# Kernel optimization log

Measured on AMD Instinct MI355X. Metric: run time of the kernel, lower is better.

Reference implementation:

```python
import jax, jax.numpy as jnp
import numpy as np

B = 4096
D_INPUT = 20
CTX = 10
IN_DIM = CTX * (D_INPUT + 1) + D_INPUT  # 230
D_MODEL = 256
N_LAYERS = 12
D_STATE = 16
D_CONV = 4
EXPAND = 2
D_INNER = EXPAND * D_MODEL  # 512
DT_RANK = (D_MODEL + 15) // 16  # ceil(256/16) = 16


def setup_inputs() -> dict:
    key = jax.random.key(0)
    ks = jax.random.split(key, 12)
    s = lambda k, shape, scale=0.02: jax.random.normal(k, shape, jnp.float32) * scale
    A = jnp.broadcast_to(jnp.arange(1, D_STATE + 1, dtype=jnp.float32), (N_LAYERS, D_INNER, D_STATE))
    return {
        "x": jax.random.normal(ks[0], (B, IN_DIM), jnp.float32),
        "Wi": s(ks[1], (IN_DIM, D_MODEL)),
        "bi": jnp.zeros((D_MODEL,), jnp.float32),
        "in_proj_w": s(ks[2], (N_LAYERS, D_MODEL, 2 * D_INNER)),
        "conv_w": s(ks[3], (N_LAYERS, D_INNER, D_CONV), 0.3),
        "conv_b": jnp.zeros((N_LAYERS, D_INNER), jnp.float32),
        "x_proj_w": s(ks[4], (N_LAYERS, D_INNER, DT_RANK + 2 * D_STATE)),
        "dt_proj_w": s(ks[5], (N_LAYERS, DT_RANK, D_INNER), 0.1),
        "dt_proj_b": jnp.full((N_LAYERS, D_INNER), -4.6, jnp.float32),  # softplus -> small dt
        "A_log": jnp.log(A),  # S4D-real init as in mamba_ssm
        "D": jnp.ones((N_LAYERS, D_INNER), jnp.float32),
        "out_proj_w": s(ks[6], (N_LAYERS, D_INNER, D_MODEL)),
        "Wo": s(ks[7], (D_MODEL, 1)),
        "bo": jnp.zeros((1,), jnp.float32),
    }


def _mamba_block(h, in_proj, conv_w, conv_b, x_proj, dt_w, dt_b, A_log, Dp, out_proj):
    # h: (B, L, D_MODEL)
    Bn, L, _ = h.shape
    xz = h @ in_proj                       # (B, L, 2*D_INNER)
    xr, z = jnp.split(xz, 2, axis=-1)
    # causal depthwise conv1d, kernel D_CONV, left-pad D_CONV-1
    xp = jnp.pad(xr, ((0, 0), (D_CONV - 1, 0), (0, 0)))
    win = jnp.stack([xp[:, k:k + L, :] for k in range(D_CONV)], axis=-1)  # (B,L,C,K)
    xc = jnp.einsum('blck,ck->blc', win, conv_w) + conv_b
    xc = jax.nn.silu(xc)
    dbl = xc @ x_proj                      # (B, L, DT_RANK + 2*D_STATE)
    dt, Bm, Cm = jnp.split(dbl, [DT_RANK, DT_RANK + D_STATE], axis=-1)
    dt = jax.nn.softplus(dt @ dt_w + dt_b)  # (B, L, D_INNER)
    A = -jnp.exp(A_log)                     # (D_INNER, D_STATE)
    dA = jnp.exp(dt[..., None] * A)                              # (B,L,di,ds)
    dBu = dt[..., None] * Bm[:, :, None, :] * xc[..., None]      # (B,L,di,ds)

    def step(hs, inp):
        dA_t, dBu_t, C_t = inp
        hs = dA_t * hs + dBu_t             # (B, di, ds)
        y_t = jnp.einsum('bds,bs->bd', hs, C_t)
        return hs, y_t

    h0 = jnp.zeros((Bn, D_INNER, D_STATE), h.dtype)
    _, ys = jax.lax.scan(step, h0, (dA.swapaxes(0, 1), dBu.swapaxes(0, 1), Cm.swapaxes(0, 1)))
    y = ys.swapaxes(0, 1)                  # (B, L, D_INNER)
    y = y + xc * Dp
    y = y * jax.nn.silu(z)
    return y @ out_proj                    # (B, L, D_MODEL)


def reference(x, Wi, bi, in_proj_w, conv_w, conv_b, x_proj_w, dt_proj_w, dt_proj_b, A_log, D, out_proj_w, Wo, bo):
    h = (x @ Wi + bi)[:, None, :]          # (B, 1, D_MODEL) -- unsqueeze(1)
    for i in range(N_LAYERS):
        h = _mamba_block(h, in_proj_w[i], conv_w[i], conv_b[i], x_proj_w[i],
                         dt_proj_w[i], dt_proj_b[i], A_log[i], D[i], out_proj_w[i])
    h = h[:, 0, :]                         # squeeze(1)
    return h @ Wo + bo                     # (B, 1)
```

## Files before the change

kernel.cpp:

```cpp
#include <hip/hip_runtime.h>
#include <hip/hip_fp8.h>
#include <math.h>

#define NB 4096
#define IN_D 230
#define DM 256
#define NL 12
#define DST 16
#define DI 512
#define DTR 16
#define XPN 48
#define XB 528
#define HB 272

typedef __attribute__((ext_vector_type(4))) float floatx4;
typedef __attribute__((ext_vector_type(2))) float floatx2;
typedef __attribute__((ext_vector_type(2))) long long2v;
typedef __attribute__((ext_vector_type(4))) int intx4;
typedef __attribute__((ext_vector_type(8))) int intx8;

__device__ __forceinline__ float silu_f(float x) {
    return x * __builtin_amdgcn_rcpf(1.0f + __expf(-x));
}
__device__ __forceinline__ float softplus_f(float x) {
    return (x > 20.0f) ? x : __logf(1.0f + __expf(x));
}

__device__ __forceinline__ unsigned char f2fp8(float x) {
#if __has_builtin(__builtin_amdgcn_cvt_pk_fp8_f32)
    return (unsigned char)(__builtin_amdgcn_cvt_pk_fp8_f32(x, x, 0, false) & 0xff);
#else
    __hip_fp8_e4m3 t(x); return (unsigned char)t.__x;
#endif
}
__device__ __forceinline__ unsigned pk4fp8(float a, float b, float c, float d) {
    unsigned w = __builtin_amdgcn_cvt_pk_fp8_f32(a, b, 0, false);
    return __builtin_amdgcn_cvt_pk_fp8_f32(c, d, w, true);
}
template<int S>
__device__ __forceinline__ float fp8sel(unsigned w) {
    return __builtin_amdgcn_cvt_f32_fp8((int)w, S);
}

__device__ __forceinline__ unsigned f2fp4(float x) {
    float ax = fabsf(x);
    unsigned s = (x < 0.0f) ? 8u : 0u;
    unsigned m;
    if      (ax < 0.25f) m = 0;
    else if (ax < 0.75f) m = 1;
    else if (ax < 1.25f) m = 2;
    else if (ax < 1.75f) m = 3;
    else if (ax < 2.50f) m = 4;
    else if (ax < 3.50f) m = 5;
    else if (ax < 5.00f) m = 6;
    else                 m = 7;
    return s | m;
}

__global__ __launch_bounds__(256) void pack_all(
    const float* __restrict__ x,
    const float* __restrict__ Wi, const float* __restrict__ ip,
    const float* __restrict__ op, const float* __restrict__ xp,
    const float* __restrict__ dtw,
    const float* __restrict__ cw, const float* __restrict__ cb,
    const float* __restrict__ db, const float* __restrict__ Dv,
    unsigned char* __restrict__ xpad,
    unsigned char* __restrict__ WiT, unsigned char* __restrict__ dtwP,
    unsigned char* __restrict__ ip4, unsigned char* __restrict__ op4,
    unsigned char* __restrict__ xp4,
    floatx2* __restrict__ cwcb, floatx2* __restrict__ dbdv)
{
    __shared__ float tbuf[64][65];
    const int fid = blockIdx.x;

    if (fid < 1264) {
        const float* src; unsigned char* dst;
        int K, N, ngK, t;
        bool isfp4;
        if (fid < 16) {
            src = Wi; dst = WiT; K = IN_D; N = DM; ngK = 4; t = fid; isfp4 = false;
        } else if (fid < 784) {
            int local = fid - 16; int l = local >> 6; t = local & 63;
            K = DM; N = 2 * DI; ngK = 4; isfp4 = true;
            src = ip + (size_t)l * K * N; dst = ip4 + (size_t)l * 131072;
        } else if (fid < 1168) {
            int local = fid - 784; int l = local >> 5; t = local & 31;
            K = DI; N = DM; ngK = 8; isfp4 = true;
            src = op + (size_t)l * K * N; dst = op4 + (size_t)l * 65536;
        } else {
            int local = fid - 1168; int l = local >> 3; t = local & 7;
            K = DI; N = XPN; ngK = 8; isfp4 = true;
            src = xp + (size_t)l * K * N; dst = xp4 + (size_t)l * 16384;
        }
        const int g = t % ngK, nb = t / ngK;
        const int k0 = g * 64, n0 = nb * 64;
        {
            const int r = threadIdx.x >> 6, c = threadIdx.x & 63;
#pragma unroll
            for (int i = 0; i < 16; i++) {
                int kk = k0 + i * 4 + r;
                int nn = n0 + c;
                tbuf[i * 4 + r][c] = (kk < K && nn < N) ? src[(size_t)kk * N + nn] : 0.0f;
            }
        }
        __syncthreads();
        if (!isfp4) {
            const int cbi = threadIdx.x >> 6;
            const int lane = threadIdx.x & 63;
            const int q = lane >> 4, m16 = lane & 15;
            const int chunk = (nb * 4 + cbi) * ngK + g;
            union { unsigned char b[16]; intx4 v; } buf;
#pragma unroll
            for (int sub = 0; sub < 2; sub++)
#pragma unroll
                for (int byt = 0; byt < 8; byt++) {
                    int k = sub * 32 + q * 8 + byt;
                    int n = cbi * 16 + m16;
                    buf.b[sub * 8 + byt] = f2fp8(tbuf[k][n]);
                }
            *(intx4*)(dst + (size_t)chunk * 1024 + lane * 16) = buf.v;
        } else {
            const int kg = g >> 1, half = g & 1;
            const int nkg128 = ngK >> 1;
            const int cbi = threadIdx.x >> 6;
            const int rem = threadIdx.x & 63;
            const int q4loc = rem >> 5;
            const int hb = (rem >> 4) & 1;
            const int m16 = rem & 15;
            const int q4 = half * 2 + q4loc;
            const int chunk = (nb * 4 + cbi) * nkg128 + kg;
            const int kb = q4loc * 32 + hb * 16;
            const int nn = cbi * 16 + m16;
            union { unsigned u[2]; long v; } buf;
#if __has_builtin(__builtin_amdgcn_cvt_scalef32_pk_fp4_f32)
            unsigned d0 = 0, d1 = 0;
            d0 = __builtin_amdgcn_cvt_scalef32_pk_fp4_f32(d0, tbuf[kb + 0][nn] * 128.0f, tbuf[kb + 1][nn] * 128.0f, 1.0f, 0);
            d0 = __builtin_amdgcn_cvt_scalef32_pk_fp4_f32(d0, tbuf[kb + 2][nn] * 128.0f, tbuf[kb + 3][nn] * 128.0f, 1.0f, 1);
            d0 = __builtin_amdgcn_cvt_scalef32_pk_fp4_f32(d0, tbuf[kb + 4][nn] * 128.0f, tbuf[kb + 5][nn] * 128.0f, 1.0f, 2);
            d0 = __builtin_amdgcn_cvt_scalef32_pk_fp4_f32(d0, tbuf[kb + 6][nn] * 128.0f, tbuf[kb + 7][nn] * 128.0f, 1.0f, 3);
            d1 = __builtin_amdgcn_cvt_scalef32_pk_fp4_f32(d1, tbuf[kb + 8][nn] * 128.0f, tbuf[kb + 9][nn] * 128.0f, 1.0f, 0);
            d1 = __builtin_amdgcn_cvt_scalef32_pk_fp4_f32(d1, tbuf[kb + 10][nn] * 128.0f, tbuf[kb + 11][nn] * 128.0f, 1.0f, 1);
            d1 = __builtin_amdgcn_cvt_scalef32_pk_fp4_f32(d1, tbuf[kb + 12][nn] * 128.0f, tbuf[kb + 13][nn] * 128.0f, 1.0f, 2);
            d1 = __builtin_amdgcn_cvt_scalef32_pk_fp4_f32(d1, tbuf[kb + 14][nn] * 128.0f, tbuf[kb + 15][nn] * 128.0f, 1.0f, 3);
            buf.u[0] = d0; buf.u[1] = d1;
#else
            union { unsigned char b[8]; long v; } bb;
#pragma unroll
            for (int bl = 0; bl < 8; bl++) {
                unsigned ob = 0;
#pragma unroll
                for (int i = 0; i < 2; i++) {
                    float v = tbuf[kb + bl * 2 + i][nn] * 128.0f;
                    ob |= f2fp4(v) << (i * 4);
                }
                bb.b[bl] = (unsigned char)ob;
            }
            buf.v = bb.v;
#endif
            *(long*)(dst + (size_t)chunk * 1024 + (q4 * 16 + m16) * 16 + hb * 8) = buf.v;
        }
    } else if (fid < 1456) {
        int gid = (fid - 1264) * 256 + threadIdx.x;
        int idx = gid * 4;
        int l = idx >> 14;
        int r14 = idx & 16383;
        int chunk = r14 >> 9;
        int rr = r14 & 511;
        int lane = rr >> 3, byt0 = rr & 7;
        int q = lane >> 4, m16 = lane & 15;
        int col = chunk * 16 + m16;
        float v[4];
#pragma unroll
        for (int j = 0; j < 4; j++) {
            int k = q * 8 + byt0 + j;
            v[j] = (k < DTR) ? dtw[(size_t)l * DTR * DI + (size_t)k * DI + col] : 0.0f;
        }
        *(unsigned*)(dtwP + idx) = pk4fp8(v[0], v[1], v[2], v[3]);
    } else if (fid < 1480) {
        int idx = (fid - 1456) * 256 + threadIdx.x;
        floatx2 v; v.x = cw[(size_t)idx * 4 + 3]; v.y = cb[idx];
        cwcb[idx] = v;
    } else if (fid < 1504) {
        int idx = (fid - 1480) * 256 + threadIdx.x;
        floatx2 v; v.x = db[idx]; v.y = Dv[idx];
        dbdv[idx] = v;
    } else {
        int gid = (fid - 1504) * 256 + threadIdx.x;
        int r = gid >> 6, c4 = (gid & 63) * 4;
        float v[4];
#pragma unroll
        for (int j = 0; j < 4; j++) {
            int k = c4 + j;
            v[j] = (k < IN_D) ? x[(size_t)r * IN_D + k] : 0.0f;
        }
        *(unsigned*)(xpad + (size_t)gid * 4) = pk4fp8(v[0], v[1], v[2], v[3]);
    }
}

__global__ __launch_bounds__(1024) void mamba_all(
    const unsigned char* __restrict__ xpad, const unsigned char* __restrict__ WiT,
    const float* __restrict__ bi,
    const unsigned char* __restrict__ ip4, const unsigned char* __restrict__ op4,
    const unsigned char* __restrict__ xp4, const unsigned char* __restrict__ dtwP,
    const floatx2* __restrict__ cwcb, const floatx2* __restrict__ dbdv,
    const float* __restrict__ Wo, const float* __restrict__ bo,
    float* __restrict__ out)
{
    __shared__ unsigned char hs[16 * HB];
    __shared__ unsigned char xcs[16 * XB];
    __shared__ unsigned char szs[16 * XB];
    __shared__ float dbls[16 * 68];

    const int tid = threadIdx.x;
    const int w = tid >> 6, lane = tid & 63;
    const int q = lane >> 4, m16 = lane & 15;
    const int rb = blockIdx.x * 16;
    const long2v z2 = (long2v){0, 0};

    {
        floatx4 a0 = (floatx4){0.f, 0.f, 0.f, 0.f};
        floatx4 a1 = (floatx4){0.f, 0.f, 0.f, 0.f};
        const unsigned char* Bp = xpad + (size_t)(rb + m16) * DM + q * 8;
        const unsigned char* Ap = WiT + (size_t)(w * 4) * 1024 + lane * 16;
#pragma unroll
        for (int g = 0; g < 4; g++) {
            long2v a = *(const long2v*)(Ap + g * 1024);
            long bv0 = *(const long*)(Bp + (g * 2) * 32);
            long bv1 = *(const long*)(Bp + (g * 2 + 1) * 32);
            a0 = __builtin_amdgcn_mfma_f32_16x16x32_fp8_fp8(a.x, bv0, a0, 0, 0, 0);
            a1 = __builtin_amdgcn_mfma_f32_16x16x32_fp8_fp8(a.y, bv1, a1, 0, 0, 0);
        }
        a0 = a0 + a1;
        floatx4 b4 = *(const floatx4*)(bi + w * 16 + q * 4);
        *(unsigned*)(hs + m16 * HB + w * 16 + q * 4) =
            pk4fp8(a0[0] + b4[0], a0[1] + b4[1], a0[2] + b4[2], a0[3] + b4[3]);
    }
    __syncthreads();

    for (int l = 0; l < NL; l++) {
        const unsigned char* ipw = ip4 + (size_t)l * 131072;
        const unsigned char* xpw = xp4 + (size_t)l * 16384;
        const unsigned char* opw = op4 + (size_t)l * 65536;
        const unsigned char* dwp = dtwP + (size_t)l * 16384;
        const floatx2* cc = cwcb + (size_t)l * DI;
        const floatx2* dd = dbdv + (size_t)l * DI;

        long2v a2[4];
        if (w < 4) {
            const unsigned char* Ap2 = xpw + (size_t)(w * 4) * 1024 + lane * 16;
#pragma unroll
            for (int i = 0; i < 4; i++) a2[i] = *(const long2v*)(Ap2 + (size_t)i * 1024);
        }
        long w3a, w3b;
        {
            const unsigned char* Wp = dwp + (size_t)(w * 2) * 512 + lane * 8;
            w3a = *(const long*)(Wp);
            w3b = *(const long*)(Wp + 512);
        }
        long2v a4[4];
        {
            const unsigned char* Ap4 = opw + (size_t)(w * 4) * 1024 + lane * 16;
#pragma unroll
            for (int i = 0; i < 4; i++) a4[i] = *(const long2v*)(Ap4 + (size_t)i * 1024);
        }

        {
            floatx4 acc[4];
#pragma unroll
            for (int t = 0; t < 4; t++) acc[t] = (floatx4){0.f, 0.f, 0.f, 0.f};
            const unsigned char* Ap = ipw + (size_t)(w * 8) * 1024 + lane * 16;
            const unsigned char* Br = hs + m16 * HB + q * 32;
#pragma unroll
            for (int kg = 0; kg < 2; kg++) {
                union { long2v h[2]; intx8 v; } bv;
                bv.h[0] = *(const long2v*)(Br + kg * 128);
                bv.h[1] = *(const long2v*)(Br + kg * 128 + 16);
#pragma unroll
                for (int t = 0; t < 4; t++) {
                    union { long2v h[2]; intx8 v; } av;
                    av.h[0] = *(const long2v*)(Ap + (size_t)(t * 2 + kg) * 1024);
                    av.h[1] = z2;
                    acc[t] = __builtin_amdgcn_mfma_scale_f32_16x16x128_f8f6f4(
                        av.v, bv.v, acc[t], 4, 0, 0, 120, 0, 127);
                }
            }
            if (w < 8) {
#pragma unroll
                for (int t = 0; t < 4; t++) {
                    int colb = w * 64 + t * 16 + q * 4;
                    floatx4 cA = *(const floatx4*)(cc + colb);
                    floatx4 cB = *(const floatx4*)(cc + colb + 2);
                    float v0 = silu_f(acc[t][0] * cA[0] + cA[1]);
                    float v1 = silu_f(acc[t][1] * cA[2] + cA[3]);
                    float v2 = silu_f(acc[t][2] * cB[0] + cB[1]);
                    float v3 = silu_f(acc[t][3] * cB[2] + cB[3]);
                    *(unsigned*)(xcs + m16 * XB + colb) = pk4fp8(v0, v1, v2, v3);
                }
            } else {
#pragma unroll
                for (int t = 0; t < 4; t++) {
                    int colb = (w - 8) * 64 + t * 16 + q * 4;
                    *(unsigned*)(szs + m16 * XB + colb) =
                        pk4fp8(silu_f(acc[t][0]), silu_f(acc[t][1]),
                               silu_f(acc[t][2]), silu_f(acc[t][3]));
                }
            }
        }
        __syncthreads();

        if (w < 4) {
            floatx4 acc = (floatx4){0.f, 0.f, 0.f, 0.f};
            const unsigned char* Br = xcs + m16 * XB + q * 32;
#pragma unroll
            for (int kg = 0; kg < 4; kg++) {
                union { long2v h[2]; intx8 v; } bv;
                bv.h[0] = *(const long2v*)(Br + kg * 128);
                bv.h[1] = *(const long2v*)(Br + kg * 128 + 16);
                union { long2v h[2]; intx8 v; } av;
                av.h[0] = a2[kg];
                av.h[1] = z2;
                acc = __builtin_amdgcn_mfma_scale_f32_16x16x128_f8f6f4(
                    av.v, bv.v, acc, 4, 0, 0, 120, 0, 127);
            }
            *(floatx4*)(&dbls[m16 * 68 + w * 16 + q * 4]) = acc;
        }
        __syncthreads();

        {
            const int cb0 = w * 32 + q * 4;

            const int brow = lane >> 2, bj = lane & 3;
            const float* dr0 = &dbls[brow * 68 + DTR];
            float p = dr0[bj]      * dr0[DST + bj]
                    + dr0[bj + 4]  * dr0[DST + bj + 4]
                    + dr0[bj + 8]  * dr0[DST + bj + 8]
                    + dr0[bj + 12] * dr0[DST + bj + 12];
            p += __shfl_xor(p, 1);
            p += __shfl_xor(p, 2);
            float bcv = __shfl(p, m16 * 4);

            long bfrag = 0;
            if (q < 2) {
                const float* dr = &dbls[m16 * 68 + q * 8];
                union { unsigned u[2]; long l; } uv;
                uv.u[0] = pk4fp8(dr[0], dr[1], dr[2], dr[3]);
                uv.u[1] = pk4fp8(dr[4], dr[5], dr[6], dr[7]);
                bfrag = uv.l;
            }

            floatx4 dA = *(const floatx4*)(dd + cb0);
            floatx4 dB = *(const floatx4*)(dd + cb0 + 2);
            floatx4 dC = *(const floatx4*)(dd + cb0 + 16);
            floatx4 dD = *(const floatx4*)(dd + cb0 + 18);
            floatx4 d0v = (floatx4){dA[0], dA[2], dB[0], dB[2]};
            floatx4 d1v = (floatx4){dC[0], dC[2], dD[0], dD[2]};
            floatx4 Dv0 = (floatx4){dA[1], dA[3], dB[1], dB[3]};
            floatx4 Dv1 = (floatx4){dC[1], dC[3], dD[1], dD[3]};
            d0v = __builtin_amdgcn_mfma_f32_16x16x32_fp8_fp8(w3a, bfrag, d0v, 0, 0, 0);
            d1v = __builtin_amdgcn_mfma_f32_16x16x32_fp8_fp8(w3b, bfrag, d1v, 0, 0, 0);

            const int off = m16 * XB + cb0;
            unsigned xw0 = *(const unsigned*)(xcs + off);
            unsigned zw0 = *(const unsigned*)(szs + off);
            unsigned xw1 = *(const unsigned*)(xcs + off + 16);
            unsigned zw1 = *(const unsigned*)(szs + off + 16);
            float y0[4], y1[4];
            y0[0] = (softplus_f(d0v[0]) * bcv + Dv0[0]) * fp8sel<0>(xw0) * fp8sel<0>(zw0);
            y0[1] = (softplus_f(d0v[1]) * bcv + Dv0[1]) * fp8sel<1>(xw0) * fp8sel<1>(zw0);
            y0[2] = (softplus_f(d0v[2]) * bcv + Dv0[2]) * fp8sel<2>(xw0) * fp8sel<2>(zw0);
            y0[3] = (softplus_f(d0v[3]) * bcv + Dv0[3]) * fp8sel<3>(xw0) * fp8sel<3>(zw0);
            y1[0] = (softplus_f(d1v[0]) * bcv + Dv1[0]) * fp8sel<0>(xw1) * fp8sel<0>(zw1);
            y1[1] = (softplus_f(d1v[1]) * bcv + Dv1[1]) * fp8sel<1>(xw1) * fp8sel<1>(zw1);
            y1[2] = (softplus_f(d1v[2]) * bcv + Dv1[2]) * fp8sel<2>(xw1) * fp8sel<2>(zw1);
            y1[3] = (softplus_f(d1v[3]) * bcv + Dv1[3]) * fp8sel<3>(xw1) * fp8sel<3>(zw1);
            *(unsigned*)(xcs + off)      = pk4fp8(y0[0], y0[1], y0[2], y0[3]);
            *(unsigned*)(xcs + off + 16) = pk4fp8(y1[0], y1[1], y1[2], y1[3]);
        }
        __syncthreads();

        {
            floatx4 acc = (floatx4){0.f, 0.f, 0.f, 0.f};
            const unsigned char* Br = xcs + m16 * XB + q * 32;
#pragma unroll
            for (int kg = 0; kg < 4; kg++) {
                union { long2v h[2]; intx8 v; } bv;
                bv.h[0] = *(const long2v*)(Br + kg * 128);
                bv.h[1] = *(const long2v*)(Br + kg * 128 + 16);
                union { long2v h[2]; intx8 v; } av;
                av.h[0] = a4[kg];
                av.h[1] = z2;
                acc = __builtin_amdgcn_mfma_scale_f32_16x16x128_f8f6f4(
                    av.v, bv.v, acc, 4, 0, 0, 120, 0, 127);
            }
            *(unsigned*)(hs + m16 * HB + w * 16 + q * 4) =
                pk4fp8(acc[0], acc[1], acc[2], acc[3]);
        }
        __syncthreads();
    }

    {
        unsigned hw = *(const unsigned*)(hs + w * HB + lane * 4);
        floatx4 w4 = *(const floatx4*)(Wo + lane * 4);
        float s = fp8sel<0>(hw) * w4[0] + fp8sel<1>(hw) * w4[1]
                + fp8sel<2>(hw) * w4[2] + fp8sel<3>(hw) * w4[3];
#pragma unroll
        for (int off = 32; off > 0; off >>= 1) s += __shfl_down(s, off);
        if (lane == 0) out[rb + w] = s + bo[0];
    }
}

extern "C" void kernel_launch(void* const* d_in, const int* in_sizes, int n_in,
                              void* d_out, int out_size, void* d_ws, size_t ws_size,
                              hipStream_t stream)
{
    const float* x       = (const float*)d_in[0];
    const float* Wi      = (const float*)d_in[1];
    const float* bi      = (const float*)d_in[2];
    const float* in_proj = (const float*)d_in[3];
    const float* conv_w  = (const float*)d_in[4];
    const float* conv_b  = (const float*)d_in[5];
    const float* x_proj  = (const float*)d_in[6];
    const float* dt_w    = (const float*)d_in[7];
    const float* dt_b    = (const float*)d_in[8];
    const float* Dp      = (const float*)d_in[10];
    const float* out_pw  = (const float*)d_in[11];
    const float* Wo      = (const float*)d_in[12];
    const float* bo      = (const float*)d_in[13];

    unsigned char* ws = (unsigned char*)d_ws;
    unsigned char* xpad = ws;
    unsigned char* WiT  = xpad + (size_t)NB * DM;
    unsigned char* dtwP = WiT + (size_t)DM * DM;
    floatx2* cwcb = (floatx2*)(dtwP + (size_t)NL * 16384);
    floatx2* dbdv = cwcb + (size_t)NL * DI;
    unsigned char* ip4 = (unsigned char*)(dbdv + (size_t)NL * DI);
    unsigned char* op4 = ip4 + (size_t)NL * 131072;
    unsigned char* xp4 = op4 + (size_t)NL * 65536;

    pack_all<<<dim3(2528), dim3(256), 0, stream>>>(
        x, Wi, in_proj, out_pw, x_proj, dt_w, conv_w, conv_b, dt_b, Dp,
        xpad, WiT, dtwP, ip4, op4, xp4, cwcb, dbdv);

    mamba_all<<<dim3(NB / 16), dim3(1024), 0, stream>>>(
        xpad, WiT, bi, ip4, op4, xp4, dtwP,
        cwcb, dbdv, Wo, bo, (float*)d_out);
}
```

Measured before the change: 168.6 us.

## Compute x_proj redundantly in every wave to drop a shared-memory barrier

Every wave now runs the full x_proj MFMA (dt, B and C tiles) itself, not just four waves writing to a shared dbls buffer. The B·C dot product and the dt fragment are formed with cross-lane shuffles, which removes the dbls scratch buffer and one __syncthreads per layer. The y output goes to szs so waves still reading xcs are not overwritten. Separately, the pack kernel's transpose now loads with float4 vectors and pads the tile row to 68. The cost is 12 MFMAs per wave where 4 waves did 4, plus more register and weight-load pressure.

New measurement: 177.4 us. +5.2%, slower.

```diff
diff --git a/kernel.cpp b/kernel.cpp
--- a/kernel.cpp
+++ b/kernel.cpp
@@ -70,7 +70,7 @@
     unsigned char* __restrict__ xp4,
     floatx2* __restrict__ cwcb, floatx2* __restrict__ dbdv)
 {
-    __shared__ float tbuf[64][65];
+    __shared__ float tbuf[64][68];
     const int fid = blockIdx.x;
 
     if (fid < 1264) {
@@ -95,12 +95,22 @@
         const int g = t % ngK, nb = t / ngK;
         const int k0 = g * 64, n0 = nb * 64;
         {
-            const int r = threadIdx.x >> 6, c = threadIdx.x & 63;
-#pragma unroll
-            for (int i = 0; i < 16; i++) {
-                int kk = k0 + i * 4 + r;
-                int nn = n0 + c;
-                tbuf[i * 4 + r][c] = (kk < K && nn < N) ? src[(size_t)kk * N + nn] : 0.0f;
+            const int t4 = threadIdx.x;
+#pragma unroll
+            for (int i = 0; i < 4; i++) {
+                int fi = i * 256 + t4;
+                int lr = fi >> 4;
+                int lc = (fi & 15) * 4;
+                int kk = k0 + lr, nn = n0 + lc;
+                floatx4 v;
+                if (kk < K && nn + 3 < N) {
+                    v = *(const floatx4*)(src + (size_t)kk * N + nn);
+                } else {
+#pragma unroll
+                    for (int j = 0; j < 4; j++)
+                        v[j] = (kk < K && nn + j < N) ? src[(size_t)kk * N + nn + j] : 0.0f;
+                }
+                *(floatx4*)(&tbuf[lr][lc]) = v;
             }
         }
         __syncthreads();
@@ -209,7 +219,6 @@
     __shared__ unsigned char hs[16 * HB];
     __shared__ unsigned char xcs[16 * XB];
     __shared__ unsigned char szs[16 * XB];
-    __shared__ float dbls[16 * 68];
 
     const int tid = threadIdx.x;
     const int w = tid >> 6, lane = tid & 63;
@@ -245,11 +254,11 @@
         const floatx2* cc = cwcb + (size_t)l * DI;
         const floatx2* dd = dbdv + (size_t)l * DI;
 
-        long2v a2[4];
-        if (w < 4) {
-            const unsigned char* Ap2 = xpw + (size_t)(w * 4) * 1024 + lane * 16;
-#pragma unroll
-            for (int i = 0; i < 4; i++) a2[i] = *(const long2v*)(Ap2 + (size_t)i * 1024);
+        long2v a2[12];
+        {
+            const unsigned char* Ap2 = xpw + (size_t)lane * 16;
+#pragma unroll
+            for (int i = 0; i < 12; i++) a2[i] = *(const long2v*)(Ap2 + (size_t)i * 1024);
         }
         long w3a, w3b;
         {
@@ -308,8 +317,10 @@
         }
         __syncthreads();
 
-        if (w < 4) {
-            floatx4 acc = (floatx4){0.f, 0.f, 0.f, 0.f};
+        {
+            floatx4 t0 = (floatx4){0.f, 0.f, 0.f, 0.f};
+            floatx4 t1 = (floatx4){0.f, 0.f, 0.f, 0.f};
+            floatx4 t2 = (floatx4){0.f, 0.f, 0.f, 0.f};
             const unsigned char* Br = xcs + m16 * XB + q * 32;
 #pragma unroll
             for (int kg = 0; kg < 4; kg++) {
@@ -317,37 +328,33 @@
                 bv.h[0] = *(const long2v*)(Br + kg * 128);
                 bv.h[1] = *(const long2v*)(Br + kg * 128 + 16);
                 union { long2v h[2]; intx8 v; } av;
-                av.h[0] = a2[kg];
                 av.h[1] = z2;
-                acc = __builtin_amdgcn_mfma_scale_f32_16x16x128_f8f6f4(
-                    av.v, bv.v, acc, 4, 0, 0, 120, 0, 127);
-            }
-            *(floatx4*)(&dbls[m16 * 68 + w * 16 + q * 4]) = acc;
-        }
-        __syncthreads();
-
-        {
-            const int cb0 = w * 32 + q * 4;
-
-            const int brow = lane >> 2, bj = lane & 3;
-            const float* dr0 = &dbls[brow * 68 + DTR];
-            float p = dr0[bj]      * dr0[DST + bj]
-                    + dr0[bj + 4]  * dr0[DST + bj + 4]
-                    + dr0[bj + 8]  * dr0[DST + bj + 8]
-                    + dr0[bj + 12] * dr0[DST + bj + 12];
-            p += __shfl_xor(p, 1);
-            p += __shfl_xor(p, 2);
-            float bcv = __shfl(p, m16 * 4);
-
+                av.h[0] = a2[0 + kg];
+                t0 = __builtin_amdgcn_mfma_scale_f32_16x16x128_f8f6f4(
+                    av.v, bv.v, t0, 4, 0, 0, 120, 0, 127);
+                av.h[0] = a2[4 + kg];
+                t1 = __builtin_amdgcn_mfma_scale_f32_16x16x128_f8f6f4(
+                    av.v, bv.v, t1, 4, 0, 0, 120, 0, 127);
+                av.h[0] = a2[8 + kg];
+                t2 = __builtin_amdgcn_mfma_scale_f32_16x16x128_f8f6f4(
+                    av.v, bv.v, t2, 4, 0, 0, 120, 0, 127);
+            }
+            float p = t1[0] * t2[0] + t1[1] * t2[1] + t1[2] * t2[2] + t1[3] * t2[3];
+            p += __shfl_xor(p, 16);
+            p += __shfl_xor(p, 32);
+            const float bcv = p;
+
+            unsigned dtq = pk4fp8(t0[0], t0[1], t0[2], t0[3]);
+            unsigned u0 = __shfl(dtq, q * 32 + m16);
+            unsigned u1 = __shfl(dtq, q * 32 + 16 + m16);
             long bfrag = 0;
             if (q < 2) {
-                const float* dr = &dbls[m16 * 68 + q * 8];
                 union { unsigned u[2]; long l; } uv;
-                uv.u[0] = pk4fp8(dr[0], dr[1], dr[2], dr[3]);
-                uv.u[1] = pk4fp8(dr[4], dr[5], dr[6], dr[7]);
+                uv.u[0] = u0; uv.u[1] = u1;
                 bfrag = uv.l;
             }
 
+            const int cb0 = w * 32 + q * 4;
             floatx4 dA = *(const floatx4*)(dd + cb0);
             floatx4 dB = *(const floatx4*)(dd + cb0 + 2);
             floatx4 dC = *(const floatx4*)(dd + cb0 + 16);
@@ -373,14 +380,14 @@
             y1[1] = (softplus_f(d1v[1]) * bcv + Dv1[1]) * fp8sel<1>(xw1) * fp8sel<1>(zw1);
             y1[2] = (softplus_f(d1v[2]) * bcv + Dv1[2]) * fp8sel<2>(xw1) * fp8sel<2>(zw1);
             y1[3] = (softplus_f(d1v[3]) * bcv + Dv1[3]) * fp8sel<3>(xw1) * fp8sel<3>(zw1);
-            *(unsigned*)(xcs + off)      = pk4fp8(y0[0], y0[1], y0[2], y0[3]);
-            *(unsigned*)(xcs + off + 16) = pk4fp8(y1[0], y1[1], y1[2], y1[3]);
+            *(unsigned*)(szs + off)      = pk4fp8(y0[0], y0[1], y0[2], y0[3]);
+            *(unsigned*)(szs + off + 16) = pk4fp8(y1[0], y1[1], y1[2], y1[3]);
         }
         __syncthreads();
 
         {
             floatx4 acc = (floatx4){0.f, 0.f, 0.f, 0.f};
-            const unsigned char* Br = xcs + m16 * XB + q * 32;
+            const unsigned char* Br = szs + m16 * XB + q * 32;
 #pragma unroll
             for (int kg = 0; kg < 4; kg++) {
                 union { long2v h[2]; intx8 v; } bv;
```
